# Kernel optimization log

Hardware: AMD Instinct MI355X
Metric: run time of the kernel (lower is better)

## Reference

```python
import jax, jax.numpy as jnp
import numpy as np

EMBED_DIM = 1024
NUM_HEADS = 16
HEAD_DIM = EMBED_DIM // NUM_HEADS


def setup_inputs() -> dict:
    key = jax.random.key(0)
    ks = jax.random.split(key, 9)
    B, S, D = 2, 2048, EMBED_DIM
    scale = 1.0 / np.sqrt(D)
    x = jax.random.normal(ks[0], (B, S, D), dtype=jnp.float32)
    # nn.Linear weights are [out, in]; store as [in, out] for x @ W
    Wq = jax.random.uniform(ks[1], (D, D), jnp.float32, -scale, scale)
    bq = jax.random.uniform(ks[2], (D,), jnp.float32, -scale, scale)
    Wk = jax.random.uniform(ks[3], (D, D), jnp.float32, -scale, scale)
    bk = jax.random.uniform(ks[4], (D,), jnp.float32, -scale, scale)
    Wv = jax.random.uniform(ks[5], (D, D), jnp.float32, -scale, scale)
    bv = jax.random.uniform(ks[6], (D,), jnp.float32, -scale, scale)
    Wo = jax.random.uniform(ks[7], (D, D), jnp.float32, -scale, scale)
    bo = jax.random.uniform(ks[8], (D,), jnp.float32, -scale, scale)
    return {"x": x, "Wq": Wq, "bq": bq, "Wk": Wk, "bk": bk,
            "Wv": Wv, "bv": bv, "Wo": Wo, "bo": bo}


def reference(x, Wq, bq, Wk, bk, Wv, bv, Wo, bo):
    B, S, D = x.shape
    H, Dh = NUM_HEADS, HEAD_DIM
    q = (x @ Wq + bq).reshape(B, S, H, Dh).transpose(0, 2, 1, 3)  # [B,H,S,Dh]
    k = (x @ Wk + bk).reshape(B, S, H, Dh).transpose(0, 2, 1, 3)
    v = (x @ Wv + bv).reshape(B, S, H, Dh).transpose(0, 2, 1, 3)
    scores = jnp.einsum('bhqd,bhkd->bhqk', q, k) / jnp.sqrt(jnp.float32(Dh))
    attn = jax.nn.softmax(scores, axis=-1)
    out = jnp.einsum('bhqk,bhkd->bhqd', attn, v)  # [B,H,S,Dh]
    out = out.transpose(0, 2, 1, 3).reshape(B, S, D)
    return out @ Wo + bo
```

## Files before the change

### kernel.cpp

```cpp
#include <hip/hip_runtime.h>
#include <hip/hip_bf16.h>
#include <stdint.h>

using f32x4 = __attribute__((ext_vector_type(4))) float;
using s16x8 = __attribute__((ext_vector_type(8))) short;
using s16x4 = __attribute__((ext_vector_type(4))) short;

__device__ __forceinline__ unsigned short f2bf(float f) {
  union { float f; unsigned int u; } v; v.f = f;
  return (unsigned short)((v.u + 0x7FFFu + ((v.u >> 16) & 1u)) >> 16);
}

__device__ __forceinline__ float exp2_(float x) {
  float r;
  asm("v_exp_f32 %0, %1" : "=v"(r) : "v"(x));
  return r;
}

__device__ __forceinline__ unsigned cvtpk(float a, float b) {
  unsigned r;
  asm("v_cvt_pk_bf16_f32 %0, %1, %2" : "=v"(r) : "v"(a), "v"(b));
  return r;
}

__device__ __forceinline__ short pbf(float f) {
  __hip_bfloat16 h = __float2bfloat16(f);
  return *(short*)&h;
}

#define GLD16(gp, lp) __builtin_amdgcn_global_load_lds( \
    (const __attribute__((address_space(1))) unsigned int*)(uintptr_t)(gp), \
    (__attribute__((address_space(3))) unsigned int*)(uintptr_t)(lp), 16, 0, 0)

__device__ __forceinline__ f32x4 mfma32(s16x8 a, s16x8 b, f32x4 c) {
  return __builtin_amdgcn_mfma_f32_16x16x32_bf16(a, b, c, 0, 0, 0);
}

__global__ __launch_bounds__(256)
void prep(const float* __restrict__ x,
          const float* __restrict__ Wq, const float* __restrict__ Wk,
          const float* __restrict__ Wv, const float* __restrict__ Wo,
          unsigned short* __restrict__ xb, unsigned short* __restrict__ Wt) {
  __shared__ float tile[64][65];
  int blk = blockIdx.x;
  int tid = threadIdx.x;
  if (blk < 1024) {
    const float4* xi = (const float4*)x;
    ushort4* xo = (ushort4*)xb;
    #pragma unroll
    for (int j = 0; j < 4; ++j) {
      int i = blk * 1024 + j * 256 + tid;
      float4 v = xi[i];
      ushort4 o;
      o.x = f2bf(v.x); o.y = f2bf(v.y); o.z = f2bf(v.z); o.w = f2bf(v.w);
      xo[i] = o;
    }
  } else {
    int wid = blk - 1024;
    int which = wid >> 8, t = wid & 255;
    const float* W = (which == 0) ? Wq : (which == 1) ? Wk : (which == 2) ? Wv : Wo;
    unsigned short* dst = Wt + (size_t)which * 1048576;
    int k0 = (t & 15) * 64, n0 = (t >> 4) * 64;
    int tx = tid & 63, ty = tid >> 6;
    #pragma unroll
    for (int j = 0; j < 64; j += 4)
      tile[ty + j][tx] = W[(size_t)(k0 + ty + j) * 1024 + n0 + tx];
    __syncthreads();
    #pragma unroll
    for (int j = 0; j < 64; j += 4)
      dst[(size_t)(n0 + ty + j) * 1024 + k0 + tx] = f2bf(tile[tx][ty + j]);
  }
}

__global__ __launch_bounds__(512, 2)
void qkv_gemm(const unsigned short* __restrict__ A,
              const unsigned short* __restrict__ Bt,
              const float* __restrict__ bq, const float* __restrict__ bk,
              const float* __restrict__ bv,
              unsigned short* __restrict__ qo, unsigned short* __restrict__ kf,
              unsigned short* __restrict__ vf) {
  __shared__ unsigned short lds2[2][28672];
  int orig = blockIdx.x;
  int wg = (orig & 7) * 32 + (orig >> 3);
  int bm = wg >> 4, bn = wg & 15;
  int m0 = bm << 8;
  int n0 = bn * 192;
  int tid = threadIdx.x;
  int w = tid >> 6, ln = tid & 63;
  int g = ln >> 4, c = ln & 15;
  int wm = w >> 2, wn = w & 3;

  int rrs = tid >> 3;
  int lcol = (((tid & 7) ^ ((tid >> 3) & 7)) << 4);
  const char* pA = (const char*)A + (size_t)(m0 + rrs) * 2048 + lcol;
  const char* pB = (const char*)Bt + (size_t)(n0 + rrs) * 2048 + lcol;
  int woff = w * 1024;

#define QKV_STAGE(buf, kt)                                                     \
  {                                                                            \
    char* db = (char*)&lds2[buf][0];                                           \
    _Pragma("unroll")                                                          \
    for (int s = 0; s < 4; ++s)                                                \
      GLD16(pA + (size_t)s * 131072 + (kt) * 128, db + s * 8192 + woff);       \
    _Pragma("unroll")                                                          \
    for (int s = 0; s < 3; ++s)                                                \
      GLD16(pB + (size_t)s * 131072 + (kt) * 128,                              \
            db + 32768 + s * 8192 + woff);                                     \
  }

  int cs = (c & 7) << 4;
#define DSFA(LA, mi, kk)                                                       \
  (*(const s16x8*)&(LA)[((mi) >> 2) * 4096 + (((mi) & 3) * 16 + c) * 64 +      \
                        ((((kk) * 64 + g * 16) ^ cs) >> 1)])
#define DSFB(LB, ni, kk)                                                       \
  (*(const s16x8*)&(LB)[((wn * 48 + (ni) * 16) >> 6) * 4096 +                  \
                        (((wn * 48 + (ni) * 16) & 63) + c) * 64 +              \
                        ((((kk) * 64 + g * 16) ^ cs) >> 1)])

  f32x4 acc[8][3];
  f32x4 zero = {0.f, 0.f, 0.f, 0.f};
  #pragma unroll
  for (int mi = 0; mi < 8; ++mi)
    #pragma unroll
    for (int ni = 0; ni < 3; ++ni) acc[mi][ni] = zero;

  QKV_STAGE(0, 0);
  asm volatile("s_waitcnt vmcnt(0)" ::: "memory");
  __builtin_amdgcn_s_barrier();

  for (int kt = 0; kt < 16; ++kt) {
    int bsel = kt & 1;
    const unsigned short* LA = &lds2[bsel][wm * 8192];
    const unsigned short* LB = &lds2[bsel][16384];
    if (kt < 15) QKV_STAGE(bsel ^ 1, kt + 1);

    s16x8 bfr[3][2];
    #pragma unroll
    for (int ni = 0; ni < 3; ++ni) {
      bfr[ni][0] = DSFB(LB, ni, 0);
      bfr[ni][1] = DSFB(LB, ni, 1);
    }
    s16x8 a[4][2];
    #pragma unroll
    for (int mi = 0; mi < 4; ++mi) {
      a[mi][0] = DSFA(LA, mi, 0);
      a[mi][1] = DSFA(LA, mi, 1);
    }
    __builtin_amdgcn_s_setprio(1);
    #pragma unroll
    for (int mi = 0; mi < 4; ++mi)
      #pragma unroll
      for (int ni = 0; ni < 3; ++ni) {
        acc[mi][ni] = mfma32(a[mi][0], bfr[ni][0], acc[mi][ni]);
        acc[mi][ni] = mfma32(a[mi][1], bfr[ni][1], acc[mi][ni]);
      }
    __builtin_amdgcn_s_setprio(0);
    #pragma unroll
    for (int mi = 0; mi < 4; ++mi) {
      a[mi][0] = DSFA(LA, mi + 4, 0);
      a[mi][1] = DSFA(LA, mi + 4, 1);
    }
    __builtin_amdgcn_s_setprio(1);
    #pragma unroll
    for (int mi = 0; mi < 4; ++mi)
      #pragma unroll
      for (int ni = 0; ni < 3; ++ni) {
        acc[mi + 4][ni] = mfma32(a[mi][0], bfr[ni][0], acc[mi + 4][ni]);
        acc[mi + 4][ni] = mfma32(a[mi][1], bfr[ni][1], acc[mi + 4][ni]);
      }
    __builtin_amdgcn_s_setprio(0);

    asm volatile("s_waitcnt vmcnt(0)" ::: "memory");
    __builtin_amdgcn_s_barrier();
  }
#undef QKV_STAGE
#undef DSFA
#undef DSFB

  #pragma unroll
  for (int ni = 0; ni < 3; ++ni) {
    int cg = n0 + wn * 48 + ni * 16 + c;
    int p = cg >> 10;
    int d = cg & 1023;
    int hh = d >> 6, dh = d & 63;
    const float* bp = (p == 0) ? bq : (p == 1) ? bk : bv;
    float bias = bp[d];
    #pragma unroll
    for (int mi = 0; mi < 8; ++mi) {
      int r = m0 + wm * 128 + mi * 16 + g * 4;
      int b2 = r >> 11, s = r & 2047;
      size_t pv = (size_t)((b2 << 4) + hh);
      if (p == 2) {
        int ch = s >> 5;
        int l16 = ((s >> 3) & 3) * 16 + (dh & 15);
        int jo = s & 7;
        ushort4 pk;
        pk.x = f2bf(acc[mi][ni][0] + bias);
        pk.y = f2bf(acc[mi][ni][1] + bias);
        pk.z = f2bf(acc[mi][ni][2] + bias);
        pk.w = f2bf(acc[mi][ni][3] + bias);
        *(ushort4*)&vf[pv * 131072 +
                       (size_t)((ch * 4 + (dh >> 4)) * 64 + l16) * 8 + jo] = pk;
      } else if (p == 1) {
        int T = s >> 4;
        int h2 = dh >> 5, gp = (dh >> 3) & 3, j = dh & 7;
        unsigned short* kd = kf + pv * 131072 + T * 1024 + h2 * 512 +
                             (gp * 16 + (s & 15)) * 8 + j;
        kd[0]  = f2bf(acc[mi][ni][0] + bias);
        kd[8]  = f2bf(acc[mi][ni][1] + bias);
        kd[16] = f2bf(acc[mi][ni][2] + bias);
        kd[24] = f2bf(acc[mi][ni][3] + bias);
      } else {
        const float sc = 0.180336880111120f;
        size_t base = (pv * 2048 + s) * 64 + dh;
        qo[base]       = f2bf((acc[mi][ni][0] + bias) * sc);
        qo[base + 64]  = f2bf((acc[mi][ni][1] + bias) * sc);
        qo[base + 128] = f2bf((acc[mi][ni][2] + bias) * sc);
        qo[base + 192] = f2bf((acc[mi][ni][3] + bias) * sc);
      }
    }
  }
}

__global__ __launch_bounds__(256, 2)
void attn_fwd(const unsigned short* __restrict__ q,
              const unsigned short* __restrict__ kfb,
              const unsigned short* __restrict__ vfb,
              unsigned short* __restrict__ ao) {
  __shared__ unsigned short ldsKV[3][8192];
  __shared__ unsigned short ldsP[4][2048];
  int orig = blockIdx.x;
  int wg = (orig & 7) * 64 + (orig >> 3);
  int pair = wg >> 4, qt = wg & 15;
  int tid = threadIdx.x;
  int w = tid >> 6, ln = tid & 63;
  int g = ln >> 4, c = ln & 15;
  int q0 = qt * 128 + w * 32;
  const unsigned short* qp = q + (size_t)pair * 131072;
  const char* kbase = (const char*)(kfb + (size_t)pair * 131072);
  const char* vbase = (const char*)(vfb + (size_t)pair * 131072);

  const char* ssrc = ((w < 2) ? kbase : vbase) + (w & 1) * 4096;
  int dsto = (w >= 2 ? 8192 : 0) + (w & 1) * 4096;

  unsigned short* Pw = &ldsP[w][0];
  int pwbase = (2 * 0 + (g >> 1)) * 128 + c * 8 + (g & 1) * 4;

  s16x8 qf[2][2];
  #pragma unroll
  for (int j = 0; j < 2; ++j)
    #pragma unroll
    for (int h = 0; h < 2; ++h)
      qf[j][h] = *(const s16x8*)&qp[(q0 + j * 16 + c) * 64 + h * 32 + g * 8];

  f32x4 acc[2][4];
  f32x4 zero = {0.f, 0.f, 0.f, 0.f};
  #pragma unroll
  for (int j = 0; j < 2; ++j)
    #pragma unroll
    for (int dt = 0; dt < 4; ++dt) acc[j][dt] = zero;
  float l0 = 0.f, l1 = 0.f;

  #pragma unroll
  for (int j = 0; j < 4; ++j)
    GLD16(ssrc + j * 1024 + ln * 16, (char*)&ldsKV[0][0] + dsto + j * 1024);

  const unsigned short* L0 = ldsKV[0];
  const unsigned short* L1 = ldsKV[1];
  const unsigned short* L2 = ldsKV[2];

#define ATTN_ITER(T, LC, LP, LN)                                               \
  {                                                                            \
    if ((T) < 31) {                                                            \
      const char* s2 = ssrc + ((T) + 1) * 8192;                                \
      char* d2 = (char*)(LN) + dsto;                                           \
      _Pragma("unroll")                                                        \
      for (int j = 0; j < 4; ++j)                                              \
        GLD16(s2 + j * 1024 + ln * 16, d2 + j * 1024);                         \
      asm volatile("s_waitcnt vmcnt(4)" ::: "memory");                         \
    } else {                                                                   \
      asm volatile("s_waitcnt vmcnt(0)" ::: "memory");                         \
    }                                                                          \
    __builtin_amdgcn_s_barrier();                                              \
    s16x8 kc[4][2];                                                            \
    _Pragma("unroll")                                                          \
    for (int kt = 0; kt < 4; ++kt) {                                           \
      kc[kt][0] = *(const s16x8*)&(LC)[kt * 1024 + ln * 8];                    \
      kc[kt][1] = *(const s16x8*)&(LC)[kt * 1024 + 512 + ln * 8];              \
    }                                                                          \
    f32x4 st[4][2];                                                            \
    __builtin_amdgcn_s_setprio(1);                                             \
    _Pragma("unroll")                                                          \
    for (int kt = 0; kt < 4; ++kt)                                             \
      _Pragma("unroll")                                                        \
      for (int j = 0; j < 2; ++j) {                                            \
        f32x4 t2 = zero;                                                       \
        t2 = mfma32(kc[kt][0], qf[j][0], t2);                                  \
        t2 = mfma32(kc[kt][1], qf[j][1], t2);                                  \
        st[kt][j] = t2;                                                        \
      }                                                                        \
    __builtin_amdgcn_s_setprio(0);                                             \
    if ((T) > 0) {                                                             \
      s16x8 pa00 = *(const s16x8*)&Pw[ln * 8];                                 \
      s16x8 pa01 = *(const s16x8*)&Pw[512 + ln * 8];                           \
      s16x8 pa10 = *(const s16x8*)&Pw[1024 + ln * 8];                          \
      s16x8 pa11 = *(const s16x8*)&Pw[1536 + ln * 8];                          \
      __builtin_amdgcn_s_setprio(1);                                           \
      _Pragma("unroll")                                                        \
      for (int m = 0; m < 2; ++m)                                              \
        _Pragma("unroll")                                                      \
        for (int dt = 0; dt < 4; ++dt) {                                       \
          s16x8 vv = *(const s16x8*)&(LP)[4096 + m * 2048 + dt * 512 + ln * 8];\
          acc[0][dt] = mfma32(m ? pa01 : pa00, vv, acc[0][dt]);                \
          acc[1][dt] = mfma32(m ? pa11 : pa10, vv, acc[1][dt]);                \
        }                                                                      \
      __builtin_amdgcn_s_setprio(0);                                           \
    }                                                                          \
    _Pragma("unroll")                                                          \
    for (int kt = 0; kt < 4; ++kt) {                                           \
      float p00 = exp2_(st[kt][0][0]), p01 = exp2_(st[kt][0][1]);              \
      float p02 = exp2_(st[kt][0][2]), p03 = exp2_(st[kt][0][3]);              \
      float p10 = exp2_(st[kt][1][0]), p11 = exp2_(st[kt][1][1]);              \
      float p12 = exp2_(st[kt][1][2]), p13 = exp2_(st[kt][1][3]);              \
      l0 += (p00 + p01) + (p02 + p03);                                         \
      l1 += (p10 + p11) + (p12 + p13);                                         \
      int wa = (kt >> 1) * 512 + (kt & 1) * 256 + pwbase;                      \
      uint2 w0; w0.x = cvtpk(p00, p01); w0.y = cvtpk(p02, p03);                \
      *(uint2*)&Pw[wa] = w0;                                                   \
      uint2 w1; w1.x = cvtpk(p10, p11); w1.y = cvtpk(p12, p13);                \
      *(uint2*)&Pw[1024 + wa] = w1;                                            \
    }                                                                          \
    __builtin_amdgcn_s_barrier();                                              \
  }

  for (int t = 0; t < 32; t += 2) {
    ATTN_ITER(t,     L0, L2, L1);
    ATTN_ITER(t + 1, L1, L0, L2);
    const unsigned short* tmp = L2;
    L2 = L1; L1 = L0; L0 = tmp;
  }
#undef ATTN_ITER

  {
    s16x8 pa00 = *(const s16x8*)&Pw[ln * 8];
    s16x8 pa01 = *(const s16x8*)&Pw[512 + ln * 8];
    s16x8 pa10 = *(const s16x8*)&Pw[1024 + ln * 8];
    s16x8 pa11 = *(const s16x8*)&Pw[1536 + ln * 8];
    __builtin_amdgcn_s_setprio(1);
    #pragma unroll
    for (int m = 0; m < 2; ++m)
      #pragma unroll
      for (int dt = 0; dt < 4; ++dt) {
        s16x8 vv = *(const s16x8*)&L2[4096 + m * 2048 + dt * 512 + ln * 8];
        acc[0][dt] = mfma32(m ? pa01 : pa00, vv, acc[0][dt]);
        acc[1][dt] = mfma32(m ? pa11 : pa10, vv, acc[1][dt]);
      }
    __builtin_amdgcn_s_setprio(0);
  }

  l0 += __shfl_xor(l0, 16); l0 += __shfl_xor(l0, 32);
  l1 += __shfl_xor(l1, 16); l1 += __shfl_xor(l1, 32);
  float li0 = 1.f / l0, li1 = 1.f / l1;
  int b = pair >> 4, hh = pair & 15;
  #pragma unroll
  for (int e = 0; e < 4; ++e) {
    float i0 = __shfl(li0, g * 4 + e);
    float i1 = __shfl(li1, g * 4 + e);
    size_t r0 = ((size_t)(b * 2048 + q0 + g * 4 + e) * 16 + hh) * 64;
    size_t r1 = ((size_t)(b * 2048 + q0 + 16 + g * 4 + e) * 16 + hh) * 64;
    #pragma unroll
    for (int dt = 0; dt < 4; ++dt) {
      ao[r0 + dt * 16 + c] = (unsigned short)pbf(acc[0][dt][e] * i0);
      ao[r1 + dt * 16 + c] = (unsigned short)pbf(acc[1][dt][e] * i1);
    }
  }
}

__global__ __launch_bounds__(256)
void out_gemm(const unsigned short* __restrict__ A,
              const unsigned short* __restrict__ Bt,
              const float* __restrict__ bo, float* __restrict__ out) {
  __shared__ unsigned short lds[2][6144];
  int orig = blockIdx.x;
  int wg = (orig & 7) * 64 + (orig >> 3);
  int bm = wg >> 3, bn = wg & 7;
  int m0 = bm << 6, n0 = bn << 7;
  int tid = threadIdx.x;
  int w = tid >> 6, ln = tid & 63;
  int g = ln >> 4, c = ln & 15;
  int wr = w >> 1, wc = w & 1;

  const unsigned short* su[3];
  int du[3];
  #pragma unroll
  for (int i = 0; i < 3; ++i) {
    int u = 3 * w + i;
    if (u < 4) {
      su[i] = A + (size_t)(m0 + u * 16 + (ln >> 2)) * 1024 + (ln & 3) * 8;
      du[i] = u * 512;
    } else {
      int v2 = u - 4;
      su[i] = Bt + (size_t)(n0 + v2 * 16 + (ln >> 2)) * 1024 + (ln & 3) * 8;
      du[i] = 2048 + v2 * 512;
    }
  }

  f32x4 acc[2][4];
  f32x4 zero = {0.f, 0.f, 0.f, 0.f};
  #pragma unroll
  for (int m = 0; m < 2; ++m)
    #pragma unroll
    for (int n = 0; n < 4; ++n) acc[m][n] = zero;

  #pragma unroll
  for (int i = 0; i < 3; ++i) GLD16(su[i], &lds[0][du[i]]);
  __syncthreads();

  int aoff = (wr * 32 + c) * 32 + g * 8;
  int boff = 2048 + (wc * 64 + c) * 32 + g * 8;

  int cur = 0;
  for (int t = 0; t < 32; ++t) {
    if (t < 31) {
      int nb = cur ^ 1;
      #pragma unroll
      for (int i = 0; i < 3; ++i) GLD16(su[i] + (t + 1) * 32, &lds[nb][du[i]]);
    }
    s16x8 af[2], bf[4];
    #pragma unroll
    for (int m = 0; m < 2; ++m)
      af[m] = *(const s16x8*)&lds[cur][aoff + m * 512];
    #pragma unroll
    for (int n = 0; n < 4; ++n)
      bf[n] = *(const s16x8*)&lds[cur][boff + n * 512];
    #pragma unroll
    for (int m = 0; m < 2; ++m)
      #pragma unroll
      for (int n = 0; n < 4; ++n)
        acc[m][n] = mfma32(af[m], bf[n], acc[m][n]);
    __syncthreads();
    cur ^= 1;
  }

  #pragma unroll
  for (int n = 0; n < 4; ++n) {
    int cg = n0 + wc * 64 + n * 16 + c;
    float bias = bo[cg];
    #pragma unroll
    for (int m = 0; m < 2; ++m) {
      int r = m0 + wr * 32 + m * 16 + g * 4;
      out[(size_t)r * 1024 + cg] = acc[m][n][0] + bias;
      out[(size_t)(r + 1) * 1024 + cg] = acc[m][n][1] + bias;
      out[(size_t)(r + 2) * 1024 + cg] = acc[m][n][2] + bias;
      out[(size_t)(r + 3) * 1024 + cg] = acc[m][n][3] + bias;
    }
  }
}

extern "C" void kernel_launch(void* const* d_in, const int* in_sizes, int n_in,
                              void* d_out, int out_size, void* d_ws, size_t ws_size,
                              hipStream_t stream) {
  (void)in_sizes; (void)n_in; (void)out_size; (void)ws_size;
  const float* x  = (const float*)d_in[0];
  const float* Wq = (const float*)d_in[1];
  const float* bq = (const float*)d_in[2];
  const float* Wk = (const float*)d_in[3];
  const float* bk = (const float*)d_in[4];
  const float* Wv = (const float*)d_in[5];
  const float* bv = (const float*)d_in[6];
  const float* Wo = (const float*)d_in[7];
  const float* bo = (const float*)d_in[8];
  float* out = (float*)d_out;
  char* ws = (char*)d_ws;
  unsigned short* xb  = (unsigned short*)(ws);
  unsigned short* Wt  = (unsigned short*)(ws + 8388608);
  unsigned short* Wot = (unsigned short*)(ws + 14680064);
  unsigned short* qb  = (unsigned short*)(ws + 16777216);
  unsigned short* kfb = (unsigned short*)(ws + 25165824);
  unsigned short* vfb = (unsigned short*)(ws + 33554432);
  unsigned short* ao  = (unsigned short*)(ws + 41943040);

  prep<<<2048, 256, 0, stream>>>(x, Wq, Wk, Wv, Wo, xb, Wt);
  qkv_gemm<<<256, 512, 0, stream>>>(xb, Wt, bq, bk, bv, qb, kfb, vfb);
  attn_fwd<<<512, 256, 0, stream>>>(qb, kfb, vfb, ao);
  out_gemm<<<512, 256, 0, stream>>>(ao, Wot, bo, out);
}
```

Before: 103.0 us.

## Split attention KV tiles across wave pairs and double the grid

```diff
diff --git a/kernel.cpp b/kernel.cpp
--- a/kernel.cpp
+++ b/kernel.cpp
@@ -222,20 +222,21 @@
   }
 }
 
-__global__ __launch_bounds__(256, 2)
+__global__ __launch_bounds__(256, 4)
 void attn_fwd(const unsigned short* __restrict__ q,
               const unsigned short* __restrict__ kfb,
               const unsigned short* __restrict__ vfb,
               unsigned short* __restrict__ ao) {
-  __shared__ unsigned short ldsKV[3][8192];
-  __shared__ unsigned short ldsP[4][2048];
+  __shared__ unsigned short ldsKV[2][8192];
+  __shared__ unsigned short ldsP[4][1024];
   int orig = blockIdx.x;
-  int wg = (orig & 7) * 64 + (orig >> 3);
-  int pair = wg >> 4, qt = wg & 15;
+  int wg = (orig & 7) * 128 + (orig >> 3);
+  int pair = wg >> 5, qt = wg & 31;
   int tid = threadIdx.x;
   int w = tid >> 6, ln = tid & 63;
   int g = ln >> 4, c = ln & 15;
-  int q0 = qt * 128 + w * 32;
+  int wq = w >> 1, wkv = w & 1;
+  int qw = qt * 64 + wq * 32;
   const unsigned short* qp = q + (size_t)pair * 131072;
   const char* kbase = (const char*)(kfb + (size_t)pair * 131072);
   const char* vbase = (const char*)(vfb + (size_t)pair * 131072);
@@ -244,14 +245,13 @@
   int dsto = (w >= 2 ? 8192 : 0) + (w & 1) * 4096;
 
   unsigned short* Pw = &ldsP[w][0];
-  int pwbase = (2 * 0 + (g >> 1)) * 128 + c * 8 + (g & 1) * 4;
 
   s16x8 qf[2][2];
   #pragma unroll
   for (int j = 0; j < 2; ++j)
     #pragma unroll
     for (int h = 0; h < 2; ++h)
-      qf[j][h] = *(const s16x8*)&qp[(q0 + j * 16 + c) * 64 + h * 32 + g * 8];
+      qf[j][h] = *(const s16x8*)&qp[(qw + j * 16 + c) * 64 + h * 32 + g * 8];
 
   f32x4 acc[2][4];
   f32x4 zero = {0.f, 0.f, 0.f, 0.f};
@@ -262,116 +262,113 @@
   float l0 = 0.f, l1 = 0.f;
 
   #pragma unroll
-  for (int j = 0; j < 4; ++j)
-    GLD16(ssrc + j * 1024 + ln * 16, (char*)&ldsKV[0][0] + dsto + j * 1024);
-
-  const unsigned short* L0 = ldsKV[0];
-  const unsigned short* L1 = ldsKV[1];
-  const unsigned short* L2 = ldsKV[2];
-
-#define ATTN_ITER(T, LC, LP, LN)                                               \
-  {                                                                            \
-    if ((T) < 31) {                                                            \
-      const char* s2 = ssrc + ((T) + 1) * 8192;                                \
-      char* d2 = (char*)(LN) + dsto;                                           \
-      _Pragma("unroll")                                                        \
-      for (int j = 0; j < 4; ++j)                                              \
-        GLD16(s2 + j * 1024 + ln * 16, d2 + j * 1024);                         \
-      asm volatile("s_waitcnt vmcnt(4)" ::: "memory");                         \
-    } else {                                                                   \
-      asm volatile("s_waitcnt vmcnt(0)" ::: "memory");                         \
-    }                                                                          \
-    __builtin_amdgcn_s_barrier();                                              \
-    s16x8 kc[4][2];                                                            \
-    _Pragma("unroll")                                                          \
-    for (int kt = 0; kt < 4; ++kt) {                                           \
-      kc[kt][0] = *(const s16x8*)&(LC)[kt * 1024 + ln * 8];                    \
-      kc[kt][1] = *(const s16x8*)&(LC)[kt * 1024 + 512 + ln * 8];              \
-    }                                                                          \
-    f32x4 st[4][2];                                                            \
-    __builtin_amdgcn_s_setprio(1);                                             \
-    _Pragma("unroll")                                                          \
-    for (int kt = 0; kt < 4; ++kt)                                             \
-      _Pragma("unroll")                                                        \
-      for (int j = 0; j < 2; ++j) {                                            \
-        f32x4 t2 = zero;                                                       \
-        t2 = mfma32(kc[kt][0], qf[j][0], t2);                                  \
-        t2 = mfma32(kc[kt][1], qf[j][1], t2);                                  \
-        st[kt][j] = t2;                                                        \
-      }                                                                        \
-    __builtin_amdgcn_s_setprio(0);                                             \
-    if ((T) > 0) {                                                             \
-      s16x8 pa00 = *(const s16x8*)&Pw[ln * 8];                                 \
-      s16x8 pa01 = *(const s16x8*)&Pw[512 + ln * 8];                           \
-      s16x8 pa10 = *(const s16x8*)&Pw[1024 + ln * 8];                          \
-      s16x8 pa11 = *(const s16x8*)&Pw[1536 + ln * 8];                          \
-      __builtin_amdgcn_s_setprio(1);                                           \
-      _Pragma("unroll")                                                        \
-      for (int m = 0; m < 2; ++m)                                              \
-        _Pragma("unroll")                                                      \
-        for (int dt = 0; dt < 4; ++dt) {                                       \
-          s16x8 vv = *(const s16x8*)&(LP)[4096 + m * 2048 + dt * 512 + ln * 8];\
-          acc[0][dt] = mfma32(m ? pa01 : pa00, vv, acc[0][dt]);                \
-          acc[1][dt] = mfma32(m ? pa11 : pa10, vv, acc[1][dt]);                \
-        }                                                                      \
-      __builtin_amdgcn_s_setprio(0);                                           \
-    }                                                                          \
-    _Pragma("unroll")                                                          \
-    for (int kt = 0; kt < 4; ++kt) {                                           \
-      float p00 = exp2_(st[kt][0][0]), p01 = exp2_(st[kt][0][1]);              \
-      float p02 = exp2_(st[kt][0][2]), p03 = exp2_(st[kt][0][3]);              \
-      float p10 = exp2_(st[kt][1][0]), p11 = exp2_(st[kt][1][1]);              \
-      float p12 = exp2_(st[kt][1][2]), p13 = exp2_(st[kt][1][3]);              \
-      l0 += (p00 + p01) + (p02 + p03);                                         \
-      l1 += (p10 + p11) + (p12 + p13);                                         \
-      int wa = (kt >> 1) * 512 + (kt & 1) * 256 + pwbase;                      \
-      uint2 w0; w0.x = cvtpk(p00, p01); w0.y = cvtpk(p02, p03);                \
-      *(uint2*)&Pw[wa] = w0;                                                   \
-      uint2 w1; w1.x = cvtpk(p10, p11); w1.y = cvtpk(p12, p13);                \
-      *(uint2*)&Pw[1024 + wa] = w1;                                            \
-    }                                                                          \
-    __builtin_amdgcn_s_barrier();                                              \
-  }
-
-  for (int t = 0; t < 32; t += 2) {
-    ATTN_ITER(t,     L0, L2, L1);
-    ATTN_ITER(t + 1, L1, L0, L2);
-    const unsigned short* tmp = L2;
-    L2 = L1; L1 = L0; L0 = tmp;
-  }
-#undef ATTN_ITER
-
-  {
-    s16x8 pa00 = *(const s16x8*)&Pw[ln * 8];
-    s16x8 pa01 = *(const s16x8*)&Pw[512 + ln * 8];
-    s16x8 pa10 = *(const s16x8*)&Pw[1024 + ln * 8];
-    s16x8 pa11 = *(const s16x8*)&Pw[1536 + ln * 8];
+  for (int jj = 0; jj < 4; ++jj)
+    GLD16(ssrc + jj * 1024 + ln * 16, (char*)&ldsKV[0][0] + dsto + jj * 1024);
+
+  int kofs = wkv * 2048;
+
+  for (int t = 0; t < 32; ++t) {
+    int buf = t & 1;
+    if (t < 31) {
+      const char* s2 = ssrc + (size_t)(t + 1) * 8192;
+      char* d2 = (char*)&ldsKV[buf ^ 1][0] + dsto;
+      #pragma unroll
+      for (int jj = 0; jj < 4; ++jj)
+        GLD16(s2 + jj * 1024 + ln * 16, d2 + jj * 1024);
+      asm volatile("s_waitcnt vmcnt(4)" ::: "memory");
+    } else {
+      asm volatile("s_waitcnt vmcnt(0)" ::: "memory");
+    }
+    __builtin_amdgcn_s_barrier();
+
+    const unsigned short* L = ldsKV[buf];
+    s16x8 kc[2][2];
+    #pragma unroll
+    for (int ktl = 0; ktl < 2; ++ktl) {
+      kc[ktl][0] = *(const s16x8*)&L[kofs + ktl * 1024 + ln * 8];
+      kc[ktl][1] = *(const s16x8*)&L[kofs + ktl * 1024 + 512 + ln * 8];
+    }
+    f32x4 st[2][2];
     __builtin_amdgcn_s_setprio(1);
     #pragma unroll
-    for (int m = 0; m < 2; ++m)
+    for (int ktl = 0; ktl < 2; ++ktl)
+      #pragma unroll
+      for (int j = 0; j < 2; ++j) {
+        f32x4 t2 = zero;
+        t2 = mfma32(kc[ktl][0], qf[j][0], t2);
+        t2 = mfma32(kc[ktl][1], qf[j][1], t2);
+        st[ktl][j] = t2;
+      }
+    __builtin_amdgcn_s_setprio(0);
+
+    s16x8 vv[4];
+    #pragma unroll
+    for (int dt = 0; dt < 4; ++dt)
+      vv[dt] = *(const s16x8*)&L[4096 + wkv * 2048 + dt * 512 + ln * 8];
+
+    #pragma unroll
+    for (int ktl = 0; ktl < 2; ++ktl)
+      #pragma unroll
+      for (int j = 0; j < 2; ++j) {
+        float p0 = exp2_(st[ktl][j][0]), p1 = exp2_(st[ktl][j][1]);
+        float p2 = exp2_(st[ktl][j][2]), p3 = exp2_(st[ktl][j][3]);
+        if (j == 0) l0 += (p0 + p1) + (p2 + p3);
+        else        l1 += (p0 + p1) + (p2 + p3);
+        int wa = j * 512 + (2 * ktl + (g >> 1)) * 128 + c * 8 + (g & 1) * 4;
+        uint2 ww;
+        ww.x = cvtpk(p0, p1);
+        ww.y = cvtpk(p2, p3);
+        *(uint2*)&Pw[wa] = ww;
+      }
+    s16x8 pa0 = *(const s16x8*)&Pw[ln * 8];
+    s16x8 pa1 = *(const s16x8*)&Pw[512 + ln * 8];
+
+    __builtin_amdgcn_s_setprio(1);
+    #pragma unroll
+    for (int dt = 0; dt < 4; ++dt) {
+      acc[0][dt] = mfma32(pa0, vv[dt], acc[0][dt]);
+      acc[1][dt] = mfma32(pa1, vv[dt], acc[1][dt]);
+    }
+    __builtin_amdgcn_s_setprio(0);
+
+    __builtin_amdgcn_s_barrier();
+  }
+
+  float* red = (float*)&ldsKV[0][0];
+  float* r = red + wq * 2176;
+  if (wkv == 1) {
+    #pragma unroll
+    for (int j = 0; j < 2; ++j)
+      #pragma unroll
+      for (int dt = 0; dt < 4; ++dt)
+        *(f32x4*)&r[(j * 4 + dt) * 256 + ln * 4] = acc[j][dt];
+    r[2048 + ln] = l0;
+    r[2048 + 64 + ln] = l1;
+  }
+  __syncthreads();
+  if (wkv == 0) {
+    #pragma unroll
+    for (int j = 0; j < 2; ++j)
+      #pragma unroll
+      for (int dt = 0; dt < 4; ++dt)
+        acc[j][dt] += *(const f32x4*)&r[(j * 4 + dt) * 256 + ln * 4];
+    l0 += r[2048 + ln];
+    l1 += r[2048 + 64 + ln];
+    l0 += __shfl_xor(l0, 16); l0 += __shfl_xor(l0, 32);
+    l1 += __shfl_xor(l1, 16); l1 += __shfl_xor(l1, 32);
+    float li0 = 1.f / l0, li1 = 1.f / l1;
+    int b = pair >> 4, hh = pair & 15;
+    #pragma unroll
+    for (int e = 0; e < 4; ++e) {
+      float i0 = __shfl(li0, g * 4 + e);
+      float i1 = __shfl(li1, g * 4 + e);
+      size_t r0 = ((size_t)(b * 2048 + qw + g * 4 + e) * 16 + hh) * 64;
+      size_t r1 = ((size_t)(b * 2048 + qw + 16 + g * 4 + e) * 16 + hh) * 64;
       #pragma unroll
       for (int dt = 0; dt < 4; ++dt) {
-        s16x8 vv = *(const s16x8*)&L2[4096 + m * 2048 + dt * 512 + ln * 8];
-        acc[0][dt] = mfma32(m ? pa01 : pa00, vv, acc[0][dt]);
-        acc[1][dt] = mfma32(m ? pa11 : pa10, vv, acc[1][dt]);
-      }
-    __builtin_amdgcn_s_setprio(0);
-  }
-
-  l0 += __shfl_xor(l0, 16); l0 += __shfl_xor(l0, 32);
-  l1 += __shfl_xor(l1, 16); l1 += __shfl_xor(l1, 32);
-  float li0 = 1.f / l0, li1 = 1.f / l1;
-  int b = pair >> 4, hh = pair & 15;
-  #pragma unroll
-  for (int e = 0; e < 4; ++e) {
-    float i0 = __shfl(li0, g * 4 + e);
-    float i1 = __shfl(li1, g * 4 + e);
-    size_t r0 = ((size_t)(b * 2048 + q0 + g * 4 + e) * 16 + hh) * 64;
-    size_t r1 = ((size_t)(b * 2048 + q0 + 16 + g * 4 + e) * 16 + hh) * 64;
-    #pragma unroll
-    for (int dt = 0; dt < 4; ++dt) {
-      ao[r0 + dt * 16 + c] = (unsigned short)pbf(acc[0][dt][e] * i0);
-      ao[r1 + dt * 16 + c] = (unsigned short)pbf(acc[1][dt][e] * i1);
+        ao[r0 + dt * 16 + c] = (unsigned short)pbf(acc[0][dt][e] * i0);
+        ao[r1 + dt * 16 + c] = (unsigned short)pbf(acc[1][dt][e] * i1);
+      }
     }
   }
 }
@@ -482,6 +479,6 @@
 
   prep<<<2048, 256, 0, stream>>>(x, Wq, Wk, Wv, Wo, xb, Wt);
   qkv_gemm<<<256, 512, 0, stream>>>(xb, Wt, bq, bk, bv, qb, kfb, vfb);
-  attn_fwd<<<512, 256, 0, stream>>>(qb, kfb, vfb, ao);
+  attn_fwd<<<1024, 256, 0, stream>>>(qb, kfb, vfb, ao);
   out_gemm<<<512, 256, 0, stream>>>(ao, Wot, bo, out);
 }
```

Result: slower. 105.5 us (+2.5%).
